# Kernel optimization log

Measured on AMD Instinct MI355X. Metric: run time of the kernel, lower is better.

## Reference

```python
import jax, jax.numpy as jnp
import numpy as np

EPS = 1e-3  # Keras BatchNormalization default epsilon
K = 7

def _bn(x, gamma, beta, mean, var):
    return gamma * (x - mean) * jax.lax.rsqrt(var + EPS) + beta

def setup_inputs() -> dict:
    key = jax.random.key(0)
    ks = jax.random.split(key, 4)
    B, L, Cin, F = 64, 512, 64, 128
    out_len = L - K + 1
    return {
        "x": jax.random.normal(ks[0], (B, L, Cin), jnp.float32),
        "conv_w": jax.random.normal(ks[1], (K, Cin, F), jnp.float32) * (1.0 / np.sqrt(K * Cin)),
        "conv_b": jnp.zeros((F,), jnp.float32),
        "bn1_gamma": jnp.ones((F,), jnp.float32),
        "bn1_beta": jnp.zeros((F,), jnp.float32),
        "bn1_mean": jnp.zeros((F,), jnp.float32),
        "bn1_var": jnp.ones((F,), jnp.float32),
        "local_w": jax.random.normal(ks[2], (out_len, K * F, F), jnp.float32) * (1.0 / np.sqrt(K * F)),
        "local_b": jnp.zeros((out_len, F), jnp.float32),
        "bn2_gamma": jnp.ones((F,), jnp.float32),
        "bn2_beta": jnp.zeros((F,), jnp.float32),
        "bn2_mean": jnp.zeros((F,), jnp.float32),
        "bn2_var": jnp.ones((F,), jnp.float32),
    }

def reference(x, conv_w, conv_b, bn1_gamma, bn1_beta, bn1_mean, bn1_var,
              local_w, local_b, bn2_gamma, bn2_beta, bn2_mean, bn2_var):
    # Conv1D, padding='same'  (NWC / WIO)
    y = jax.lax.conv_general_dilated(
        x, conv_w, window_strides=(1,), padding="SAME",
        dimension_numbers=("NWC", "WIO", "NWC")) + conv_b
    y = jax.nn.relu(_bn(y, bn1_gamma, bn1_beta, bn1_mean, bn1_var))

    # LocallyConnected1D, padding='valid': per-position unshared weights
    B, L, F = y.shape
    out_len = L - K + 1
    idx = jnp.arange(out_len)[:, None] + jnp.arange(K)[None, :]  # (out_len, K)
    patches = y[:, idx, :].reshape(B, out_len, K * F)             # (B, out_len, K*F)
    z = jnp.einsum("blk,lkf->blf", patches, local_w) + local_b    # (B, out_len, F)
    z = jax.nn.relu(_bn(z, bn2_gamma, bn2_beta, bn2_mean, bn2_var))
    return z
```

## Files before the change

kernel.cpp:

```cpp
#include <hip/hip_runtime.h>
#include <hip/hip_bf16.h>

typedef __attribute__((ext_vector_type(8))) short bf16x8;
typedef __attribute__((ext_vector_type(4))) float f32x4;

#define BB   64
#define LL   512
#define CIN  64
#define FF   128
#define KW   7
#define OUTL 506
#define LPAD 518
#define KC   448
#define KL   896
#define BK   32
#define NCH  28
#define EPSV 1e-3f

#define NPAD  (BB * LPAD * CIN)
#define PADB  (NPAD / 256)
#define NWT   (FF * KC)
#define WTB   (NWT / 256)

static __device__ __forceinline__ short f2bf(float f) {
    unsigned u = __builtin_bit_cast(unsigned, f);
    unsigned r = (u + 0x7fffu + ((u >> 16) & 1u)) >> 16;
    return (short)r;
}

static __device__ __forceinline__ void g2lds16(const float* g, float* l) {
    __builtin_amdgcn_global_load_lds(
        (const __attribute__((address_space(1))) unsigned int*)g,
        (__attribute__((address_space(3))) unsigned int*)l, 16, 0, 0);
}

__global__ void prep_kernel(const float* __restrict__ x, const float* __restrict__ w,
                            short* __restrict__ xp, short* __restrict__ wt) {
    if (blockIdx.x < PADB) {
        int i = blockIdx.x * 256 + threadIdx.x;
        int c  = i & (CIN - 1);
        int t  = i >> 6;
        int lp = t % LPAD;
        int b  = t / LPAD;
        float v = 0.0f;
        int l = lp - 3;
        if (l >= 0 && l < LL) v = x[(b * LL + l) * CIN + c];
        xp[i] = f2bf(v);
    } else {
        int i = (blockIdx.x - PADB) * 256 + threadIdx.x;
        int n = i / KC;
        int k = i - n * KC;
        wt[i] = f2bf(w[(size_t)k * FF + n]);
    }
}

__global__ __launch_bounds__(256) void conv_bn_kernel(
    const short* __restrict__ xp, const short* __restrict__ wt,
    const float* __restrict__ cb, const float* __restrict__ g,
    const float* __restrict__ be, const float* __restrict__ mu,
    const float* __restrict__ va, short* __restrict__ y) {
    const int lane = threadIdx.x & 63;
    const int wid  = threadIdx.x >> 6;
    const int m0   = blockIdx.x * 64;
    const int nb   = wid * 32;
    const int q    = lane >> 4;
    const int ln   = lane & 15;

    const short* arow[4];
#pragma unroll
    for (int mt = 0; mt < 4; ++mt) {
        int m = m0 + mt * 16 + ln;
        int b = m >> 9, l = m & 511;
        arow[mt] = xp + (b * LPAD + l) * CIN;
    }
    const short* brow[2];
#pragma unroll
    for (int nt = 0; nt < 2; ++nt)
        brow[nt] = wt + (size_t)(nb + nt * 16 + ln) * KC;

    f32x4 acc[4][2];
#pragma unroll
    for (int mt = 0; mt < 4; ++mt)
#pragma unroll
        for (int nt = 0; nt < 2; ++nt) acc[mt][nt] = (f32x4){0.f, 0.f, 0.f, 0.f};

#pragma unroll 2
    for (int kc = 0; kc < KC; kc += 32) {
        const int ko = kc + q * 8;
        bf16x8 a[4], bf[2];
#pragma unroll
        for (int mt = 0; mt < 4; ++mt) a[mt] = *(const bf16x8*)(arow[mt] + ko);
#pragma unroll
        for (int nt = 0; nt < 2; ++nt) bf[nt] = *(const bf16x8*)(brow[nt] + ko);
#pragma unroll
        for (int mt = 0; mt < 4; ++mt)
#pragma unroll
            for (int nt = 0; nt < 2; ++nt)
                acc[mt][nt] = __builtin_amdgcn_mfma_f32_16x16x32_bf16(
                    a[mt], bf[nt], acc[mt][nt], 0, 0, 0);
    }

#pragma unroll
    for (int nt = 0; nt < 2; ++nt) {
        const int n = nb + nt * 16 + ln;
        const float s  = g[n] * rsqrtf(va[n] + EPSV);
        const float b2 = s * (cb[n] - mu[n]) + be[n];
#pragma unroll
        for (int mt = 0; mt < 4; ++mt) {
            const int mbase = m0 + mt * 16 + q * 4;
#pragma unroll
            for (int r = 0; r < 4; ++r) {
                float v = fmaxf(acc[mt][nt][r] * s + b2, 0.0f);
                y[(size_t)(mbase + r) * FF + n] = f2bf(v);
            }
        }
    }
}

__global__ __launch_bounds__(256) void local_bn_kernel(
    const short* __restrict__ y, const float* __restrict__ lw,
    const float* __restrict__ lb, const float* __restrict__ g,
    const float* __restrict__ be, const float* __restrict__ mu,
    const float* __restrict__ va, float* __restrict__ out) {
    __shared__ float wtile[2][BK * FF];
    const int l    = blockIdx.x;
    const int lane = threadIdx.x & 63;
    const int wid  = threadIdx.x >> 6;
    const int nb   = wid * 32;
    const int q    = lane >> 4;
    const int ln   = lane & 15;

    const float* wl = lw + (size_t)l * (KL * FF);

    const short* arow[4];
#pragma unroll
    for (int mt = 0; mt < 4; ++mt)
        arow[mt] = y + (size_t)(mt * 16 + ln) * (LL * FF) + (size_t)l * FF;

    f32x4 acc[4][2];
#pragma unroll
    for (int mt = 0; mt < 4; ++mt)
#pragma unroll
        for (int nt = 0; nt < 2; ++nt) acc[mt][nt] = (f32x4){0.f, 0.f, 0.f, 0.f};

    {
        const float* src = wl;
#pragma unroll
        for (int r = 0; r < 4; ++r)
            g2lds16(src + (size_t)(r * 256 + wid * 64 + lane) * 4,
                    &wtile[0][(r * 256 + wid * 64) * 4]);
    }

    for (int c = 0; c < NCH; ++c) {
        __syncthreads();
        if (c + 1 < NCH) {
            const float* src = wl + (size_t)(c + 1) * (BK * FF);
            float* dst = wtile[(c + 1) & 1];
#pragma unroll
            for (int r = 0; r < 4; ++r)
                g2lds16(src + (size_t)(r * 256 + wid * 64 + lane) * 4,
                        &dst[(r * 256 + wid * 64) * 4]);
        }
        const float* wb = wtile[c & 1];
        const int ko = c * BK + q * 8;

        bf16x8 a[4];
#pragma unroll
        for (int mt = 0; mt < 4; ++mt) a[mt] = *(const bf16x8*)(arow[mt] + ko);

        bf16x8 bf[2];
#pragma unroll
        for (int nt = 0; nt < 2; ++nt) {
            const int n = nb + nt * 16 + ln;
#pragma unroll
            for (int j = 0; j < 8; ++j)
                bf[nt][j] = f2bf(wb[(q * 8 + j) * FF + n]);
        }
#pragma unroll
        for (int mt = 0; mt < 4; ++mt)
#pragma unroll
            for (int nt = 0; nt < 2; ++nt)
                acc[mt][nt] = __builtin_amdgcn_mfma_f32_16x16x32_bf16(
                    a[mt], bf[nt], acc[mt][nt], 0, 0, 0);
    }

#pragma unroll
    for (int nt = 0; nt < 2; ++nt) {
        const int n = nb + nt * 16 + ln;
        const float s  = g[n] * rsqrtf(va[n] + EPSV);
        const float b2 = s * (lb[(size_t)l * FF + n] - mu[n]) + be[n];
#pragma unroll
        for (int mt = 0; mt < 4; ++mt) {
            const int bbase = mt * 16 + q * 4;
#pragma unroll
            for (int r = 0; r < 4; ++r) {
                float v = fmaxf(acc[mt][nt][r] * s + b2, 0.0f);
                out[(size_t)(bbase + r) * (OUTL * FF) + (size_t)l * FF + n] = v;
            }
        }
    }
}

extern "C" void kernel_launch(void* const* d_in, const int* in_sizes, int n_in,
                              void* d_out, int out_size, void* d_ws, size_t ws_size,
                              hipStream_t stream) {
    const float* x       = (const float*)d_in[0];
    const float* conv_w  = (const float*)d_in[1];
    const float* conv_b  = (const float*)d_in[2];
    const float* bn1_g   = (const float*)d_in[3];
    const float* bn1_b   = (const float*)d_in[4];
    const float* bn1_m   = (const float*)d_in[5];
    const float* bn1_v   = (const float*)d_in[6];
    const float* local_w = (const float*)d_in[7];
    const float* local_b = (const float*)d_in[8];
    const float* bn2_g   = (const float*)d_in[9];
    const float* bn2_b   = (const float*)d_in[10];
    const float* bn2_m   = (const float*)d_in[11];
    const float* bn2_v   = (const float*)d_in[12];
    float* out = (float*)d_out;

    short* xp  = (short*)d_ws;
    short* ybf = xp + (size_t)NPAD;
    short* wt  = ybf + (size_t)BB * LL * FF;

    prep_kernel<<<PADB + WTB, 256, 0, stream>>>(x, conv_w, xp, wt);
    conv_bn_kernel<<<(BB * LL) / 64, 256, 0, stream>>>(
        xp, wt, conv_b, bn1_g, bn1_b, bn1_m, bn1_v, ybf);
    local_bn_kernel<<<OUTL, 256, 0, stream>>>(
        ybf, local_w, local_b, bn2_g, bn2_b, bn2_m, bn2_v, out);
}
```

Baseline: 374.8 us.

## Fuse prep, conv and locally-connected stages into one cooperative persistent kernel

```diff
diff --git a/kernel.cpp b/kernel.cpp
--- a/kernel.cpp
+++ b/kernel.cpp
@@ -1,5 +1,8 @@
 #include <hip/hip_runtime.h>
 #include <hip/hip_bf16.h>
+#include <hip/hip_cooperative_groups.h>
+
+namespace cg = cooperative_groups;
 
 typedef __attribute__((ext_vector_type(8))) short bf16x8;
 typedef __attribute__((ext_vector_type(4))) float f32x4;
@@ -22,6 +25,9 @@
 #define NWT   (FF * KC)
 #define WTB   (NWT / 256)
 
+#define GRID  512
+#define NTHR  (GRID * 256)
+
 static __device__ __forceinline__ short f2bf(float f) {
     unsigned u = __builtin_bit_cast(unsigned, f);
     unsigned r = (u + 0x7fffu + ((u >> 16) & 1u)) >> 16;
@@ -33,6 +39,179 @@
         (const __attribute__((address_space(1))) unsigned int*)g,
         (__attribute__((address_space(3))) unsigned int*)l, 16, 0, 0);
 }
+
+__global__ __launch_bounds__(256, 2) void fused_kernel(
+    const float* __restrict__ x, const float* __restrict__ conv_w,
+    const float* __restrict__ conv_b,
+    const float* __restrict__ bn1_g, const float* __restrict__ bn1_b,
+    const float* __restrict__ bn1_m, const float* __restrict__ bn1_v,
+    const float* __restrict__ local_w, const float* __restrict__ local_b,
+    const float* __restrict__ bn2_g, const float* __restrict__ bn2_b,
+    const float* __restrict__ bn2_m, const float* __restrict__ bn2_v,
+    float* __restrict__ out,
+    short* __restrict__ xp, short* __restrict__ ybf, short* __restrict__ wt)
+{
+    __shared__ float wtile[2][BK * FF];
+    const int tid  = threadIdx.x;
+    const int bid  = blockIdx.x;
+    const int lane = tid & 63;
+    const int wid  = tid >> 6;
+    const int q    = lane >> 4;
+    const int ln   = lane & 15;
+
+    for (int i = bid * 256 + tid; i < NPAD; i += NTHR) {
+        int c  = i & (CIN - 1);
+        int t  = i >> 6;
+        int lp = t % LPAD;
+        int b  = t / LPAD;
+        float v = 0.0f;
+        int l = lp - 3;
+        if (l >= 0 && l < LL) v = x[(b * LL + l) * CIN + c];
+        xp[i] = f2bf(v);
+    }
+    for (int i = bid * 256 + tid; i < NWT; i += NTHR) {
+        int n = i / KC;
+        int k = i - n * KC;
+        wt[i] = f2bf(conv_w[(size_t)k * FF + n]);
+    }
+
+    __threadfence();
+    cg::this_grid().sync();
+
+    {
+        const int m0 = bid * 64;
+        const int nb = wid * 32;
+
+        const short* arow[4];
+#pragma unroll
+        for (int mt = 0; mt < 4; ++mt) {
+            int m = m0 + mt * 16 + ln;
+            int b = m >> 9, l = m & 511;
+            arow[mt] = xp + (b * LPAD + l) * CIN;
+        }
+        const short* brow[2];
+#pragma unroll
+        for (int nt = 0; nt < 2; ++nt)
+            brow[nt] = wt + (size_t)(nb + nt * 16 + ln) * KC;
+
+        f32x4 acc[4][2];
+#pragma unroll
+        for (int mt = 0; mt < 4; ++mt)
+#pragma unroll
+            for (int nt = 0; nt < 2; ++nt) acc[mt][nt] = (f32x4){0.f, 0.f, 0.f, 0.f};
+
+#pragma unroll 2
+        for (int kc = 0; kc < KC; kc += 32) {
+            const int ko = kc + q * 8;
+            bf16x8 a[4], bf[2];
+#pragma unroll
+            for (int mt = 0; mt < 4; ++mt) a[mt] = *(const bf16x8*)(arow[mt] + ko);
+#pragma unroll
+            for (int nt = 0; nt < 2; ++nt) bf[nt] = *(const bf16x8*)(brow[nt] + ko);
+#pragma unroll
+            for (int mt = 0; mt < 4; ++mt)
+#pragma unroll
+                for (int nt = 0; nt < 2; ++nt)
+                    acc[mt][nt] = __builtin_amdgcn_mfma_f32_16x16x32_bf16(
+                        a[mt], bf[nt], acc[mt][nt], 0, 0, 0);
+        }
+
+#pragma unroll
+        for (int nt = 0; nt < 2; ++nt) {
+            const int n = nb + nt * 16 + ln;
+            const float s  = bn1_g[n] * rsqrtf(bn1_v[n] + EPSV);
+            const float b2 = s * (conv_b[n] - bn1_m[n]) + bn1_b[n];
+#pragma unroll
+            for (int mt = 0; mt < 4; ++mt) {
+                const int mbase = m0 + mt * 16 + q * 4;
+#pragma unroll
+                for (int r = 0; r < 4; ++r) {
+                    float v = fmaxf(acc[mt][nt][r] * s + b2, 0.0f);
+                    ybf[(size_t)(mbase + r) * FF + n] = f2bf(v);
+                }
+            }
+        }
+    }
+
+    __threadfence();
+    cg::this_grid().sync();
+
+    if (bid < OUTL) {
+        const int l  = bid;
+        const int nb = wid * 32;
+
+        const float* wl = local_w + (size_t)l * (KL * FF);
+
+        const short* arow[4];
+#pragma unroll
+        for (int mt = 0; mt < 4; ++mt)
+            arow[mt] = ybf + (size_t)(mt * 16 + ln) * (LL * FF) + (size_t)l * FF;
+
+        f32x4 acc[4][2];
+#pragma unroll
+        for (int mt = 0; mt < 4; ++mt)
+#pragma unroll
+            for (int nt = 0; nt < 2; ++nt) acc[mt][nt] = (f32x4){0.f, 0.f, 0.f, 0.f};
+
+        {
+            const float* src = wl;
+#pragma unroll
+            for (int r = 0; r < 4; ++r)
+                g2lds16(src + (size_t)(r * 256 + wid * 64 + lane) * 4,
+                        &wtile[0][(r * 256 + wid * 64) * 4]);
+        }
+
+        for (int c = 0; c < NCH; ++c) {
+            __syncthreads();
+            if (c + 1 < NCH) {
+                const float* src = wl + (size_t)(c + 1) * (BK * FF);
+                float* dst = wtile[(c + 1) & 1];
+#pragma unroll
+                for (int r = 0; r < 4; ++r)
+                    g2lds16(src + (size_t)(r * 256 + wid * 64 + lane) * 4,
+                            &dst[(r * 256 + wid * 64) * 4]);
+            }
+            const float* wb = wtile[c & 1];
+            const int ko = c * BK + q * 8;
+
+            bf16x8 a[4];
+#pragma unroll
+            for (int mt = 0; mt < 4; ++mt) a[mt] = *(const bf16x8*)(arow[mt] + ko);
+
+            bf16x8 bf[2];
+#pragma unroll
+            for (int nt = 0; nt < 2; ++nt) {
+                const int n = nb + nt * 16 + ln;
+#pragma unroll
+                for (int j = 0; j < 8; ++j)
+                    bf[nt][j] = f2bf(wb[(q * 8 + j) * FF + n]);
+            }
+#pragma unroll
+            for (int mt = 0; mt < 4; ++mt)
+#pragma unroll
+                for (int nt = 0; nt < 2; ++nt)
+                    acc[mt][nt] = __builtin_amdgcn_mfma_f32_16x16x32_bf16(
+                        a[mt], bf[nt], acc[mt][nt], 0, 0, 0);
+        }
+
+#pragma unroll
+        for (int nt = 0; nt < 2; ++nt) {
+            const int n = nb + nt * 16 + ln;
+            const float s  = bn2_g[n] * rsqrtf(bn2_v[n] + EPSV);
+            const float b2 = s * (local_b[(size_t)l * FF + n] - bn2_m[n]) + bn2_b[n];
+#pragma unroll
+            for (int mt = 0; mt < 4; ++mt) {
+                const int bbase = mt * 16 + q * 4;
+#pragma unroll
+                for (int r = 0; r < 4; ++r) {
+                    float v = fmaxf(acc[mt][nt][r] * s + b2, 0.0f);
+                    out[(size_t)(bbase + r) * (OUTL * FF) + (size_t)l * FF + n] = v;
+                }
+            }
+        }
+    }
+}
+
 
 __global__ void prep_kernel(const float* __restrict__ x, const float* __restrict__ w,
                             short* __restrict__ xp, short* __restrict__ wt) {
@@ -223,9 +402,21 @@
     short* ybf = xp + (size_t)NPAD;
     short* wt  = ybf + (size_t)BB * LL * FF;
 
-    prep_kernel<<<PADB + WTB, 256, 0, stream>>>(x, conv_w, xp, wt);
-    conv_bn_kernel<<<(BB * LL) / 64, 256, 0, stream>>>(
-        xp, wt, conv_b, bn1_g, bn1_b, bn1_m, bn1_v, ybf);
-    local_bn_kernel<<<OUTL, 256, 0, stream>>>(
-        ybf, local_w, local_b, bn2_g, bn2_b, bn2_m, bn2_v, out);
-}
+    void* args[] = {
+        (void*)&x, (void*)&conv_w, (void*)&conv_b,
+        (void*)&bn1_g, (void*)&bn1_b, (void*)&bn1_m, (void*)&bn1_v,
+        (void*)&local_w, (void*)&local_b,
+        (void*)&bn2_g, (void*)&bn2_b, (void*)&bn2_m, (void*)&bn2_v,
+        (void*)&out, (void*)&xp, (void*)&ybf, (void*)&wt
+    };
+    hipError_t err = hipLaunchCooperativeKernel(
+        (void*)fused_kernel, dim3(GRID), dim3(256), args, 0, stream);
+
+    if (err != hipSuccess) {
+        prep_kernel<<<PADB + WTB, 256, 0, stream>>>(x, conv_w, xp, wt);
+        conv_bn_kernel<<<(BB * LL) / 64, 256, 0, stream>>>(
+            xp, wt, conv_b, bn1_g, bn1_b, bn1_m, bn1_v, ybf);
+        local_bn_kernel<<<OUTL, 256, 0, stream>>>(
+            ybf, local_w, local_b, bn2_g, bn2_b, bn2_m, bn2_v, out);
+    }
+}
```

New measurement: 596.5 us. +59.1%, slower.

## Split local-connected GEMM across two N-halves per position with swizzled LDS tiles

Applied to the files above, without the earlier changes.

```diff
diff --git a/kernel.cpp b/kernel.cpp
--- a/kernel.cpp
+++ b/kernel.cpp
@@ -13,8 +13,8 @@
 #define LPAD 518
 #define KC   448
 #define KL   896
-#define BK   32
-#define NCH  28
+#define BK2  64
+#define NCH2 14
 #define EPSV 1e-3f
 
 #define NPAD  (BB * LPAD * CIN)
@@ -122,81 +122,78 @@
     const float* __restrict__ lb, const float* __restrict__ g,
     const float* __restrict__ be, const float* __restrict__ mu,
     const float* __restrict__ va, float* __restrict__ out) {
-    __shared__ float wtile[2][BK * FF];
-    const int l    = blockIdx.x;
+    __shared__ float wtile[2][BK2 * 64];
+    const int l    = blockIdx.x >> 1;
+    const int h    = blockIdx.x & 1;
     const int lane = threadIdx.x & 63;
     const int wid  = threadIdx.x >> 6;
-    const int nb   = wid * 32;
     const int q    = lane >> 4;
     const int ln   = lane & 15;
-
-    const float* wl = lw + (size_t)l * (KL * FF);
+    const int nl   = wid * 16 + ln;
+
+    const float* wlh = lw + (size_t)l * (KL * FF) + h * 64;
 
     const short* arow[4];
 #pragma unroll
     for (int mt = 0; mt < 4; ++mt)
         arow[mt] = y + (size_t)(mt * 16 + ln) * (LL * FF) + (size_t)l * FF;
 
-    f32x4 acc[4][2];
-#pragma unroll
-    for (int mt = 0; mt < 4; ++mt)
-#pragma unroll
-        for (int nt = 0; nt < 2; ++nt) acc[mt][nt] = (f32x4){0.f, 0.f, 0.f, 0.f};
-
-    {
-        const float* src = wl;
-#pragma unroll
-        for (int r = 0; r < 4; ++r)
-            g2lds16(src + (size_t)(r * 256 + wid * 64 + lane) * 4,
-                    &wtile[0][(r * 256 + wid * 64) * 4]);
-    }
-
-    for (int c = 0; c < NCH; ++c) {
+    f32x4 acc[4];
+#pragma unroll
+    for (int mt = 0; mt < 4; ++mt) acc[mt] = (f32x4){0.f, 0.f, 0.f, 0.f};
+
+#define STAGE(kc_, buf_)                                                        \
+    {                                                                           \
+        _Pragma("unroll")                                                       \
+        for (int r = 0; r < 4; ++r) {                                           \
+            const int ib   = (r * 4 + wid) * 256;                               \
+            const int e    = ib + lane * 4;                                     \
+            const int row  = e >> 6;                                            \
+            const int colp = e & 63;                                            \
+            const int col  = colp ^ (((row >> 3) & 1) << 4);                    \
+            g2lds16(wlh + (size_t)((kc_) + row) * FF + col, &(buf_)[ib]);       \
+        }                                                                       \
+    }
+
+    STAGE(0, wtile[0]);
+
+    for (int c = 0; c < NCH2; ++c) {
         __syncthreads();
-        if (c + 1 < NCH) {
-            const float* src = wl + (size_t)(c + 1) * (BK * FF);
-            float* dst = wtile[(c + 1) & 1];
-#pragma unroll
-            for (int r = 0; r < 4; ++r)
-                g2lds16(src + (size_t)(r * 256 + wid * 64 + lane) * 4,
-                        &dst[(r * 256 + wid * 64) * 4]);
+        if (c + 1 < NCH2) STAGE((c + 1) * BK2, wtile[(c + 1) & 1]);
+        const float* wb = wtile[c & 1];
+
+#pragma unroll
+        for (int s = 0; s < 2; ++s) {
+            const int ko = c * BK2 + s * 32 + q * 8;
+            bf16x8 a[4];
+#pragma unroll
+            for (int mt = 0; mt < 4; ++mt) a[mt] = *(const bf16x8*)(arow[mt] + ko);
+
+            bf16x8 bfr;
+#pragma unroll
+            for (int j = 0; j < 8; ++j) {
+                const int row = s * 32 + q * 8 + j;
+                const int col = nl ^ (((row >> 3) & 1) << 4);
+                bfr[j] = f2bf(wb[row * 64 + col]);
+            }
+#pragma unroll
+            for (int mt = 0; mt < 4; ++mt)
+                acc[mt] = __builtin_amdgcn_mfma_f32_16x16x32_bf16(
+                    a[mt], bfr, acc[mt], 0, 0, 0);
         }
-        const float* wb = wtile[c & 1];
-        const int ko = c * BK + q * 8;
-
-        bf16x8 a[4];
-#pragma unroll
-        for (int mt = 0; mt < 4; ++mt) a[mt] = *(const bf16x8*)(arow[mt] + ko);
-
-        bf16x8 bf[2];
-#pragma unroll
-        for (int nt = 0; nt < 2; ++nt) {
-            const int n = nb + nt * 16 + ln;
-#pragma unroll
-            for (int j = 0; j < 8; ++j)
-                bf[nt][j] = f2bf(wb[(q * 8 + j) * FF + n]);
-        }
-#pragma unroll
-        for (int mt = 0; mt < 4; ++mt)
-#pragma unroll
-            for (int nt = 0; nt < 2; ++nt)
-                acc[mt][nt] = __builtin_amdgcn_mfma_f32_16x16x32_bf16(
-                    a[mt], bf[nt], acc[mt][nt], 0, 0, 0);
-    }
-
-#pragma unroll
-    for (int nt = 0; nt < 2; ++nt) {
-        const int n = nb + nt * 16 + ln;
-        const float s  = g[n] * rsqrtf(va[n] + EPSV);
-        const float b2 = s * (lb[(size_t)l * FF + n] - mu[n]) + be[n];
-#pragma unroll
-        for (int mt = 0; mt < 4; ++mt) {
-            const int bbase = mt * 16 + q * 4;
-#pragma unroll
-            for (int r = 0; r < 4; ++r) {
-                float v = fmaxf(acc[mt][nt][r] * s + b2, 0.0f);
-                out[(size_t)(bbase + r) * (OUTL * FF) + (size_t)l * FF + n] = v;
-            }
+    }
+#undef STAGE
+
+    const int n = h * 64 + nl;
+    const float s  = g[n] * rsqrtf(va[n] + EPSV);
+    const float b2 = s * (lb[(size_t)l * FF + n] - mu[n]) + be[n];
+#pragma unroll
+    for (int mt = 0; mt < 4; ++mt) {
+        const int bbase = mt * 16 + q * 4;
+#pragma unroll
+        for (int r = 0; r < 4; ++r) {
+            float v = fmaxf(acc[mt][r] * s + b2, 0.0f);
+            out[(size_t)(bbase + r) * (OUTL * FF) + (size_t)l * FF + n] = v;
         }
     }
 }
@@ -226,6 +223,6 @@
     prep_kernel<<<PADB + WTB, 256, 0, stream>>>(x, conv_w, xp, wt);
     conv_bn_kernel<<<(BB * LL) / 64, 256, 0, stream>>>(
         xp, wt, conv_b, bn1_g, bn1_b, bn1_m, bn1_v, ybf);
-    local_bn_kernel<<<OUTL, 256, 0, stream>>>(
+    local_bn_kernel<<<2 * OUTL, 256, 0, stream>>>(
         ybf, local_w, local_b, bn2_g, bn2_b, bn2_m, bn2_v, out);
 }
```

Measured after the change: 380.2 us. Within noise of the previous version (+1.4%).

## Fuse input padding and weight bf16 conversion into conv kernel

Applied to the files above, without the earlier changes.

```diff
diff --git a/kernel.cpp b/kernel.cpp
--- a/kernel.cpp
+++ b/kernel.cpp
@@ -10,17 +10,14 @@
 #define FF   128
 #define KW   7
 #define OUTL 506
-#define LPAD 518
 #define KC   448
 #define KL   896
 #define BK   32
-#define NCH  28
+#define NCHC 14
+#define NCHL 28
 #define EPSV 1e-3f
 
-#define NPAD  (BB * LPAD * CIN)
-#define PADB  (NPAD / 256)
-#define NWT   (FF * KC)
-#define WTB   (NWT / 256)
+#define CONVB ((BB * LL) / 64)
 
 static __device__ __forceinline__ short f2bf(float f) {
     unsigned u = __builtin_bit_cast(unsigned, f);
@@ -34,31 +31,12 @@
         (__attribute__((address_space(3))) unsigned int*)l, 16, 0, 0);
 }
 
-__global__ void prep_kernel(const float* __restrict__ x, const float* __restrict__ w,
-                            short* __restrict__ xp, short* __restrict__ wt) {
-    if (blockIdx.x < PADB) {
-        int i = blockIdx.x * 256 + threadIdx.x;
-        int c  = i & (CIN - 1);
-        int t  = i >> 6;
-        int lp = t % LPAD;
-        int b  = t / LPAD;
-        float v = 0.0f;
-        int l = lp - 3;
-        if (l >= 0 && l < LL) v = x[(b * LL + l) * CIN + c];
-        xp[i] = f2bf(v);
-    } else {
-        int i = (blockIdx.x - PADB) * 256 + threadIdx.x;
-        int n = i / KC;
-        int k = i - n * KC;
-        wt[i] = f2bf(w[(size_t)k * FF + n]);
-    }
-}
-
 __global__ __launch_bounds__(256) void conv_bn_kernel(
-    const short* __restrict__ xp, const short* __restrict__ wt,
+    const float* __restrict__ x, const float* __restrict__ cw,
     const float* __restrict__ cb, const float* __restrict__ g,
     const float* __restrict__ be, const float* __restrict__ mu,
     const float* __restrict__ va, short* __restrict__ y) {
+    __shared__ float wchunk[2][BK * FF];
     const int lane = threadIdx.x & 63;
     const int wid  = threadIdx.x >> 6;
     const int m0   = blockIdx.x * 64;
@@ -66,17 +44,15 @@
     const int q    = lane >> 4;
     const int ln   = lane & 15;
 
-    const short* arow[4];
+    const float* xbase[4];
+    int lrow[4];
 #pragma unroll
     for (int mt = 0; mt < 4; ++mt) {
         int m = m0 + mt * 16 + ln;
         int b = m >> 9, l = m & 511;
-        arow[mt] = xp + (b * LPAD + l) * CIN;
-    }
-    const short* brow[2];
-#pragma unroll
-    for (int nt = 0; nt < 2; ++nt)
-        brow[nt] = wt + (size_t)(nb + nt * 16 + ln) * KC;
+        lrow[mt]  = l;
+        xbase[mt] = x + (long)((b << 9) + l - 3) * CIN;
+    }
 
     f32x4 acc[4][2];
 #pragma unroll
@@ -84,14 +60,46 @@
 #pragma unroll
         for (int nt = 0; nt < 2; ++nt) acc[mt][nt] = (f32x4){0.f, 0.f, 0.f, 0.f};
 
-#pragma unroll 2
-    for (int kc = 0; kc < KC; kc += 32) {
-        const int ko = kc + q * 8;
-        bf16x8 a[4], bf[2];
-#pragma unroll
-        for (int mt = 0; mt < 4; ++mt) a[mt] = *(const bf16x8*)(arow[mt] + ko);
-#pragma unroll
-        for (int nt = 0; nt < 2; ++nt) bf[nt] = *(const bf16x8*)(brow[nt] + ko);
+#define STAGEW(kc_, buf_)                                                      \
+    {                                                                          \
+        _Pragma("unroll")                                                      \
+        for (int r = 0; r < 4; ++r) {                                          \
+            const int ib = (r * 4 + wid) * 256;                                \
+            g2lds16(cw + (size_t)(kc_) * FF + ib + lane * 4, &(buf_)[ib]);     \
+        }                                                                      \
+    }
+
+    STAGEW(0, wchunk[0]);
+
+    for (int c = 0; c < NCHC; ++c) {
+        __syncthreads();
+        if (c + 1 < NCHC) STAGEW((c + 1) * BK, wchunk[(c + 1) & 1]);
+        const float* wb = wchunk[c & 1];
+
+        const int ko = c * BK + q * 8;
+        const int kw = ko >> 6;
+
+        bf16x8 a[4];
+#pragma unroll
+        for (int mt = 0; mt < 4; ++mt) {
+            const bool v = (unsigned)(lrow[mt] - 3 + kw) < (unsigned)LL;
+            f32x4 lo = v ? *(const f32x4*)(xbase[mt] + ko)     : (f32x4){0.f, 0.f, 0.f, 0.f};
+            f32x4 hi = v ? *(const f32x4*)(xbase[mt] + ko + 4) : (f32x4){0.f, 0.f, 0.f, 0.f};
+#pragma unroll
+            for (int j = 0; j < 4; ++j) {
+                a[mt][j]     = f2bf(lo[j]);
+                a[mt][j + 4] = f2bf(hi[j]);
+            }
+        }
+
+        bf16x8 bf[2];
+#pragma unroll
+        for (int nt = 0; nt < 2; ++nt) {
+            const int n = nb + nt * 16 + ln;
+#pragma unroll
+            for (int j = 0; j < 8; ++j)
+                bf[nt][j] = f2bf(wb[(q * 8 + j) * FF + n]);
+        }
 #pragma unroll
         for (int mt = 0; mt < 4; ++mt)
 #pragma unroll
@@ -99,6 +107,7 @@
                 acc[mt][nt] = __builtin_amdgcn_mfma_f32_16x16x32_bf16(
                     a[mt], bf[nt], acc[mt][nt], 0, 0, 0);
     }
+#undef STAGEW
 
 #pragma unroll
     for (int nt = 0; nt < 2; ++nt) {
@@ -151,9 +160,9 @@
                     &wtile[0][(r * 256 + wid * 64) * 4]);
     }
 
-    for (int c = 0; c < NCH; ++c) {
+    for (int c = 0; c < NCHL; ++c) {
         __syncthreads();
-        if (c + 1 < NCH) {
+        if (c + 1 < NCHL) {
             const float* src = wl + (size_t)(c + 1) * (BK * FF);
             float* dst = wtile[(c + 1) & 1];
 #pragma unroll
@@ -219,13 +228,10 @@
     const float* bn2_v   = (const float*)d_in[12];
     float* out = (float*)d_out;
 
-    short* xp  = (short*)d_ws;
-    short* ybf = xp + (size_t)NPAD;
-    short* wt  = ybf + (size_t)BB * LL * FF;
-
-    prep_kernel<<<PADB + WTB, 256, 0, stream>>>(x, conv_w, xp, wt);
-    conv_bn_kernel<<<(BB * LL) / 64, 256, 0, stream>>>(
-        xp, wt, conv_b, bn1_g, bn1_b, bn1_m, bn1_v, ybf);
+    short* ybf = (short*)d_ws;
+
+    conv_bn_kernel<<<CONVB, 256, 0, stream>>>(
+        x, conv_w, conv_b, bn1_g, bn1_b, bn1_m, bn1_v, ybf);
     local_bn_kernel<<<OUTL, 256, 0, stream>>>(
         ybf, local_w, local_b, bn2_g, bn2_b, bn2_m, bn2_v, out);
 }
```

Measured after the change: 380.6 us. About the same (+1.5%).
